# Kernel tuning notes

Measured on AMD Instinct MI355X. Metric: run time of the kernel, lower is better.

Reference implementation:

```python
import jax, jax.numpy as jnp
import numpy as np
import math

D_MODEL = 768
H = 12
D_K = D_MODEL // H


def setup_inputs() -> dict:
    key = jax.random.key(0)
    ks = jax.random.split(key, 12)
    B, S = 2, 2048
    q = jax.random.normal(ks[0], (B, S, D_MODEL), dtype=jnp.float32)
    k = jax.random.normal(ks[1], (B, S, D_MODEL), dtype=jnp.float32)
    v = jax.random.normal(ks[2], (B, S, D_MODEL), dtype=jnp.float32)
    mask = jax.random.randint(ks[3], (1, 1, S, S), 0, 2, dtype=jnp.int32)
    scale = 1.0 / math.sqrt(D_MODEL)
    w_q = jax.random.normal(ks[4], (D_MODEL, D_MODEL), dtype=jnp.float32) * scale
    b_q = jnp.zeros((D_MODEL,), dtype=jnp.float32)
    w_k = jax.random.normal(ks[5], (D_MODEL, D_MODEL), dtype=jnp.float32) * scale
    b_k = jnp.zeros((D_MODEL,), dtype=jnp.float32)
    w_v = jax.random.normal(ks[6], (D_MODEL, D_MODEL), dtype=jnp.float32) * scale
    b_v = jnp.zeros((D_MODEL,), dtype=jnp.float32)
    w_o = jax.random.normal(ks[7], (D_MODEL, D_MODEL), dtype=jnp.float32) * scale
    b_o = jnp.zeros((D_MODEL,), dtype=jnp.float32)
    return {"q": q, "k": k, "v": v, "mask": mask,
            "w_q": w_q, "b_q": b_q, "w_k": w_k, "b_k": b_k,
            "w_v": w_v, "b_v": b_v, "w_o": w_o, "b_o": b_o}


def reference(q, k, v, mask, w_q, b_q, w_k, b_k, w_v, b_v, w_o, b_o):
    B, S, _ = q.shape
    # torch nn.Linear: y = x @ W^T + b
    qp = (q @ w_q.T + b_q).reshape(B, S, H, D_K).transpose(0, 2, 1, 3)  # [B,H,S,Dk]
    kp = (k @ w_k.T + b_k).reshape(B, S, H, D_K).transpose(0, 2, 1, 3)
    vp = (v @ w_v.T + b_v).reshape(B, S, H, D_K).transpose(0, 2, 1, 3)
    # full [B,H,S,S] score matrix (the memory-bound round-trip)
    scores = jnp.einsum('bhqd,bhkd->bhqk', qp, kp) / math.sqrt(D_K)
    scores = jnp.where(mask == 0, jnp.float32(-1e9), scores)
    attn = jax.nn.softmax(scores, axis=-1)
    x = jnp.einsum('bhqk,bhkd->bhqd', attn, vp)  # [B,H,S,Dk]
    x = x.transpose(0, 2, 1, 3).reshape(B, S, H * D_K)
    return x @ w_o.T + b_o
```

## Files before the change

### kernel.cpp

```cpp
#include <hip/hip_runtime.h>
#include <hip/hip_bf16.h>

typedef __attribute__((ext_vector_type(8))) __bf16 bf16x8;
typedef __attribute__((ext_vector_type(8))) short short8;
typedef __attribute__((ext_vector_type(4))) float f32x4;
typedef __attribute__((ext_vector_type(4))) ushort us4;

#define LOG2E 1.44269504088896f

static __device__ __forceinline__ ushort f2bf(float f) {
  union { float f; unsigned u; } x; x.f = f;
  unsigned r = x.u + 0x7fffu + ((x.u >> 16) & 1u);
  return (ushort)(r >> 16);
}

static __device__ __forceinline__ void gll16(const ushort* g, ushort* l) {
  __builtin_amdgcn_global_load_lds(
      (const __attribute__((address_space(1))) unsigned*)g,
      (__attribute__((address_space(3))) unsigned*)l, 16, 0, 0);
}

#define NQ 3145728u
#define NW 589824u
__global__ __launch_bounds__(256)
void cvt_all(const float* __restrict__ q, const float* __restrict__ k,
             const float* __restrict__ v,
             const float* __restrict__ wq, const float* __restrict__ wk,
             const float* __restrict__ wv, const float* __restrict__ wo,
             ushort* __restrict__ dst)
{
  size_t i = ((size_t)blockIdx.x * 256 + threadIdx.x) * 4;
  const float* src; size_t off;
  if (i < NQ)            { src = q; off = i; }
  else if (i < 2u * NQ)  { src = k; off = i - NQ; }
  else if (i < 3u * NQ)  { src = v; off = i - 2u * NQ; }
  else {
    size_t j = i - 3u * NQ;
    unsigned wsel = (unsigned)(j / NW);
    off = j % NW;
    src = (wsel == 0) ? wq : (wsel == 1) ? wk : (wsel == 2) ? wv : wo;
  }
  f32x4 x = *(const f32x4*)(src + off);
  us4 o;
#pragma unroll
  for (int t = 0; t < 4; t++) o[t] = f2bf(x[t]);
  *(us4*)(dst + i) = o;
}

template<int MODE>
static __device__ __forceinline__ void gemm_core(const ushort* __restrict__ A,
                                                 const ushort* __restrict__ Wrow0,
                                                 const float* __restrict__ bias0,
                                                 void* __restrict__ outv,
                                                 int m0, int c0)
{
  constexpr int K = 768;
  __shared__ ushort As[128 * 32];
  __shared__ ushort Bs[128 * 32];
  const int tid  = threadIdx.x;
  const int lane = tid & 63;
  const int wid  = tid >> 6;
  const int wr = (wid >> 1) * 64;
  const int wc = (wid & 1) * 64;

  f32x4 acc[4][4];
#pragma unroll
  for (int i = 0; i < 4; i++)
#pragma unroll
    for (int j = 0; j < 4; j++) acc[i][j] = f32x4{0.f, 0.f, 0.f, 0.f};

  const int srow = wid * 16 + (lane >> 2);
  const int scol = (lane & 3) * 8;
  const ushort* gA0 = A     + (size_t)(m0 + srow) * K + scol;
  const ushort* gA1 = gA0 + (size_t)64 * K;
  const ushort* gB0 = Wrow0 + (size_t)srow * K + scol;
  const ushort* gB1 = gB0 + (size_t)64 * K;
  ushort* lA0 = &As[srow * 32 + scol];
  ushort* lA1 = &As[(srow + 64) * 32 + scol];
  ushort* lB0 = &Bs[srow * 32 + scol];
  ushort* lB1 = &Bs[(srow + 64) * 32 + scol];

  const int fr  = lane & 15;
  const int kg8 = (lane >> 4) * 8;

  for (int kt = 0; kt < K; kt += 32) {
    __syncthreads();
    gll16(gA0 + kt, lA0);
    gll16(gA1 + kt, lA1);
    gll16(gB0 + kt, lB0);
    gll16(gB1 + kt, lB1);
    __syncthreads();

    bf16x8 af[4], wf[4];
#pragma unroll
    for (int i = 0; i < 4; i++) af[i] = *(const bf16x8*)&As[(wr + i * 16 + fr) * 32 + kg8];
#pragma unroll
    for (int j = 0; j < 4; j++) wf[j] = *(const bf16x8*)&Bs[(wc + j * 16 + fr) * 32 + kg8];
#pragma unroll
    for (int i = 0; i < 4; i++)
#pragma unroll
      for (int j = 0; j < 4; j++)
        acc[i][j] = __builtin_amdgcn_mfma_f32_16x16x32_bf16(af[i], wf[j], acc[i][j], 0, 0, 0);
  }

#pragma unroll
  for (int i = 0; i < 4; i++) {
#pragma unroll
    for (int j = 0; j < 4; j++) {
#pragma unroll
      for (int r = 0; r < 4; r++) {
        int m  = m0 + wr + i * 16 + (lane >> 4) * 4 + r;
        int lc = wc + j * 16 + fr;
        float val = acc[i][j][r] + bias0[lc];
        if (MODE == 0) {
          int nn = c0 + lc;
          int hh = nn >> 6, dk = nn & 63;
          ((ushort*)outv)[(((size_t)(m >> 11) * 12 + hh) * 2048 + (m & 2047)) * 64 + dk] = f2bf(val);
        } else {
          ((float*)outv)[(size_t)m * 768 + c0 + lc] = val;
        }
      }
    }
  }
}

__global__ __launch_bounds__(256)
void qkv_gemm2(const ushort* __restrict__ CV,
               const float* __restrict__ bq, const float* __restrict__ bk,
               const float* __restrict__ bv,
               ushort* __restrict__ Qp, ushort* __restrict__ Kp, ushort* __restrict__ Vp)
{
  const int m0 = blockIdx.x * 128;
  const int n0 = blockIdx.y * 128;
  const int proj = n0 / 768;
  const int c0 = n0 - proj * 768;
  const ushort* A  = CV + (size_t)proj * NQ;
  const ushort* Wc = CV + (size_t)3 * NQ;
  const float* bias = (proj == 0) ? bq : (proj == 1) ? bk : bv;
  ushort* O = (proj == 0) ? Qp : (proj == 1) ? Kp : Vp;
  gemm_core<0>(A, Wc + (size_t)n0 * 768, bias + c0, O, m0, c0);
}

__global__ __launch_bounds__(256)
void o_gemm2(const ushort* __restrict__ X, const ushort* __restrict__ Wo,
             const float* __restrict__ bo, float* __restrict__ out)
{
  const int m0 = blockIdx.x * 128;
  const int n0 = blockIdx.y * 128;
  gemm_core<1>(X, Wo + (size_t)n0 * 768, bo + n0, out, m0, n0);
}

__global__ __launch_bounds__(256)
void attn_kernel(const ushort* __restrict__ Qp, const ushort* __restrict__ Kp,
                 const ushort* __restrict__ Vp, const int* __restrict__ mask,
                 ushort* __restrict__ X)
{
  constexpr int S = 2048;
  __shared__ ushort Ks[64][72];
  __shared__ ushort Vt[64][72];
  __shared__ ushort Ps[4][16][72];

  const int tid  = threadIdx.x;
  const int lane = tid & 63;
  const int w    = tid >> 6;
  const int qb   = blockIdx.x;
  const int bh   = blockIdx.y;
  const int b    = bh / 12, h = bh % 12;

  const ushort* Qb = Qp + (size_t)bh * S * 64;
  const ushort* Kb = Kp + (size_t)bh * S * 64;
  const ushort* Vb = Vp + (size_t)bh * S * 64;

  const int q0  = qb * 64;
  const int fr  = lane & 15;
  const int kg8 = (lane >> 4) * 8;

  const int qrow = q0 + w * 16 + fr;
  bf16x8 qf[2];
  qf[0] = *(const bf16x8*)&Qb[(size_t)qrow * 64 + kg8];
  qf[1] = *(const bf16x8*)&Qb[(size_t)qrow * 64 + 32 + kg8];

  float m_r[4] = {-1e9f, -1e9f, -1e9f, -1e9f};
  float l_r[4] = {0.f, 0.f, 0.f, 0.f};
  f32x4 accO[4];
#pragma unroll
  for (int ni = 0; ni < 4; ni++) accO[ni] = f32x4{0.f, 0.f, 0.f, 0.f};

  const int skey = tid >> 2;
  const int sc0  = (tid & 3) * 16;
  const size_t mrow_base = (size_t)(q0 + w * 16 + (lane >> 4) * 4) * S;

  for (int k0 = 0; k0 < S; k0 += 64) {
    short8 kv0 = *(const short8*)&Kb[(size_t)(k0 + skey) * 64 + sc0];
    short8 kv1 = *(const short8*)&Kb[(size_t)(k0 + skey) * 64 + sc0 + 8];
    short8 vv0 = *(const short8*)&Vb[(size_t)(k0 + skey) * 64 + sc0];
    short8 vv1 = *(const short8*)&Vb[(size_t)(k0 + skey) * 64 + sc0 + 8];
    __syncthreads();
    *(short8*)&Ks[skey][sc0]     = kv0;
    *(short8*)&Ks[skey][sc0 + 8] = kv1;
#pragma unroll
    for (int i = 0; i < 8; i++) {
      Vt[sc0 + i][skey]     = (ushort)vv0[i];
      Vt[sc0 + 8 + i][skey] = (ushort)vv1[i];
    }
    __syncthreads();

    f32x4 sc4[4];
#pragma unroll
    for (int ni = 0; ni < 4; ni++) {
      bf16x8 kf0 = *(const bf16x8*)&Ks[ni * 16 + fr][kg8];
      bf16x8 kf1 = *(const bf16x8*)&Ks[ni * 16 + fr][32 + kg8];
      f32x4 c = {0.f, 0.f, 0.f, 0.f};
      c = __builtin_amdgcn_mfma_f32_16x16x32_bf16(qf[0], kf0, c, 0, 0, 0);
      c = __builtin_amdgcn_mfma_f32_16x16x32_bf16(qf[1], kf1, c, 0, 0, 0);
      sc4[ni] = c;
    }

    float p[4][4];
#pragma unroll
    for (int r = 0; r < 4; r++) {
#pragma unroll
      for (int ni = 0; ni < 4; ni++) {
        int mk = mask[mrow_base + (size_t)r * S + k0 + ni * 16 + fr];
        float s = sc4[ni][r] * 0.125f;
        p[ni][r] = mk ? s : -1e9f;
      }
    }

#pragma unroll
    for (int r = 0; r < 4; r++) {
      float mx = fmaxf(fmaxf(p[0][r], p[1][r]), fmaxf(p[2][r], p[3][r]));
      mx = fmaxf(mx, __shfl_xor(mx, 1));
      mx = fmaxf(mx, __shfl_xor(mx, 2));
      mx = fmaxf(mx, __shfl_xor(mx, 4));
      mx = fmaxf(mx, __shfl_xor(mx, 8));
      float mn = fmaxf(m_r[r], mx);
      float al = exp2f((m_r[r] - mn) * LOG2E);
      m_r[r] = mn;
      float ls = 0.f;
#pragma unroll
      for (int ni = 0; ni < 4; ni++) {
        float e = exp2f((p[ni][r] - mn) * LOG2E);
        p[ni][r] = e;
        ls += e;
      }
      ls += __shfl_xor(ls, 1);
      ls += __shfl_xor(ls, 2);
      ls += __shfl_xor(ls, 4);
      ls += __shfl_xor(ls, 8);
      l_r[r] = l_r[r] * al + ls;
#pragma unroll
      for (int ni = 0; ni < 4; ni++) accO[ni][r] *= al;
    }

#pragma unroll
    for (int r = 0; r < 4; r++)
#pragma unroll
      for (int ni = 0; ni < 4; ni++)
        Ps[w][(lane >> 4) * 4 + r][ni * 16 + fr] = f2bf(p[ni][r]);

#pragma unroll
    for (int ks = 0; ks < 2; ks++) {
      bf16x8 pf = *(const bf16x8*)&Ps[w][fr][ks * 32 + kg8];
#pragma unroll
      for (int ni = 0; ni < 4; ni++) {
        bf16x8 vf = *(const bf16x8*)&Vt[ni * 16 + fr][ks * 32 + kg8];
        accO[ni] = __builtin_amdgcn_mfma_f32_16x16x32_bf16(pf, vf, accO[ni], 0, 0, 0);
      }
    }
  }

#pragma unroll
  for (int ni = 0; ni < 4; ni++) {
#pragma unroll
    for (int r = 0; r < 4; r++) {
      int qq = q0 + w * 16 + (lane >> 4) * 4 + r;
      float o = accO[ni][r] / l_r[r];
      X[((size_t)b * S + qq) * 768 + h * 64 + ni * 16 + fr] = f2bf(o);
    }
  }
}

extern "C" void kernel_launch(void* const* d_in, const int* in_sizes, int n_in,
                              void* d_out, int out_size, void* d_ws, size_t ws_size,
                              hipStream_t stream) {
  const float* q  = (const float*)d_in[0];
  const float* k  = (const float*)d_in[1];
  const float* v  = (const float*)d_in[2];
  const int* mask = (const int*)d_in[3];
  const float* wq = (const float*)d_in[4];
  const float* bq = (const float*)d_in[5];
  const float* wk = (const float*)d_in[6];
  const float* bk = (const float*)d_in[7];
  const float* wv = (const float*)d_in[8];
  const float* bv = (const float*)d_in[9];
  const float* wo = (const float*)d_in[10];
  const float* bo = (const float*)d_in[11];
  float* out = (float*)d_out;

  ushort* CV = (ushort*)d_ws;
  ushort* Qp = CV + (size_t)3 * NQ + (size_t)4 * NW;
  ushort* Kp = Qp + NQ;
  ushort* Vp = Kp + NQ;
  ushort* Xb = Vp + NQ;

  cvt_all<<<11520, 256, 0, stream>>>(q, k, v, wq, wk, wv, wo, CV);
  qkv_gemm2<<<dim3(32, 18), dim3(256), 0, stream>>>(CV, bq, bk, bv, Qp, Kp, Vp);
  attn_kernel<<<dim3(32, 24), dim3(256), 0, stream>>>(Qp, Kp, Vp, mask, Xb);
  o_gemm2<<<dim3(32, 6), dim3(256), 0, stream>>>(Xb, CV + (size_t)3 * NQ + (size_t)3 * NW, bo, out);
}
```

Measured before the change: 278.1 us.

## Bit-pack mask, widen attention KV tile to 128 with register prefetch

Adds a mask_pack kernel that ballots the int32 mask into 64-bit words. The attention kernel then reads bits instead of int32 values, which cuts mask traffic by a large factor. The attention loop now handles 128 keys per iteration and prefetches the next K/V tile into registers while computing the current one. It also applies a lazy softmax max-rescale with an 11.5 threshold and a pre-multiplied log2 scale, uses a packed bf16 convert, and swizzles block indices so heads in the same wave of blocks share the mask. The cost is an extra kernel launch and reuse of the CV workspace for the mask buffer; this reuse is safe only because qkv_gemm2 runs before mask_pack overwrites it. The lazy rescale also changes numerics slightly.

After: 264.1 us. -5.0%, faster.

```diff
diff --git a/kernel.cpp b/kernel.cpp
--- a/kernel.cpp
+++ b/kernel.cpp
@@ -4,14 +4,20 @@
 typedef __attribute__((ext_vector_type(8))) __bf16 bf16x8;
 typedef __attribute__((ext_vector_type(8))) short short8;
 typedef __attribute__((ext_vector_type(4))) float f32x4;
-typedef __attribute__((ext_vector_type(4))) ushort us4;
 
 #define LOG2E 1.44269504088896f
+#define SCL (0.125f * 1.44269504088896f)
 
 static __device__ __forceinline__ ushort f2bf(float f) {
   union { float f; unsigned u; } x; x.f = f;
   unsigned r = x.u + 0x7fffu + ((x.u >> 16) & 1u);
   return (ushort)(r >> 16);
+}
+
+static __device__ __forceinline__ unsigned cvt_pk_bf16(float a, float b) {
+  unsigned r;
+  asm("v_cvt_pk_bf16_f32 %0, %1, %2" : "=v"(r) : "v"(a), "v"(b));
+  return r;
 }
 
 static __device__ __forceinline__ void gll16(const ushort* g, ushort* l) {
@@ -41,10 +47,20 @@
     src = (wsel == 0) ? wq : (wsel == 1) ? wk : (wsel == 2) ? wv : wo;
   }
   f32x4 x = *(const f32x4*)(src + off);
-  us4 o;
-#pragma unroll
-  for (int t = 0; t < 4; t++) o[t] = f2bf(x[t]);
-  *(us4*)(dst + i) = o;
+  uint2 o;
+  o.x = cvt_pk_bf16(x[0], x[1]);
+  o.y = cvt_pk_bf16(x[2], x[3]);
+  *(uint2*)(dst + i) = o;
+}
+
+__global__ __launch_bounds__(256)
+void mask_pack(const int* __restrict__ mask, unsigned long long* __restrict__ mb)
+{
+  size_t gw = (size_t)blockIdx.x * 4 + (threadIdx.x >> 6);
+  int lane = threadIdx.x & 63;
+  int mk = mask[gw * 64 + lane];
+  unsigned long long bits = __ballot(mk != 0);
+  if (lane == 0) mb[gw] = bits;
 }
 
 template<int MODE>
@@ -150,22 +166,24 @@
   gemm_core<1>(X, Wo + (size_t)n0 * 768, bo + n0, out, m0, n0);
 }
 
-__global__ __launch_bounds__(256)
+__global__ __launch_bounds__(256, 3)
 void attn_kernel(const ushort* __restrict__ Qp, const ushort* __restrict__ Kp,
-                 const ushort* __restrict__ Vp, const int* __restrict__ mask,
+                 const ushort* __restrict__ Vp,
+                 const unsigned long long* __restrict__ mb,
                  ushort* __restrict__ X)
 {
   constexpr int S = 2048;
-  __shared__ ushort Ks[64][72];
-  __shared__ ushort Vt[64][72];
-  __shared__ ushort Ps[4][16][72];
+  __shared__ ushort Ks[128][72];
+  __shared__ ushort Vt[64][136];
+  __shared__ ushort Ps[4][16][136];
 
   const int tid  = threadIdx.x;
   const int lane = tid & 63;
   const int w    = tid >> 6;
-  const int qb   = blockIdx.x;
-  const int bh   = blockIdx.y;
-  const int b    = bh / 12, h = bh % 12;
+  const int bid  = blockIdx.x;
+  const int bh = (bid & 7) + 8 * (bid >> 8);
+  const int qb = (bid >> 3) & 31;
+  const int b = bh / 12, h = bh % 12;
 
   const ushort* Qb = Qp + (size_t)bh * S * 64;
   const ushort* Kb = Kp + (size_t)bh * S * 64;
@@ -173,12 +191,13 @@
 
   const int q0  = qb * 64;
   const int fr  = lane & 15;
-  const int kg8 = (lane >> 4) * 8;
+  const int g   = lane >> 4;
+  const int kg8 = g * 8;
+  const int qrow4 = q0 + w * 16 + g * 4;
 
   const int qrow = q0 + w * 16 + fr;
-  bf16x8 qf[2];
-  qf[0] = *(const bf16x8*)&Qb[(size_t)qrow * 64 + kg8];
-  qf[1] = *(const bf16x8*)&Qb[(size_t)qrow * 64 + 32 + kg8];
+  bf16x8 qf0 = *(const bf16x8*)&Qb[(size_t)qrow * 64 + kg8];
+  bf16x8 qf1 = *(const bf16x8*)&Qb[(size_t)qrow * 64 + 32 + kg8];
 
   float m_r[4] = {-1e9f, -1e9f, -1e9f, -1e9f};
   float l_r[4] = {0.f, 0.f, 0.f, 0.f};
@@ -188,79 +207,104 @@
 
   const int skey = tid >> 2;
   const int sc0  = (tid & 3) * 16;
-  const size_t mrow_base = (size_t)(q0 + w * 16 + (lane >> 4) * 4) * S;
-
-  for (int k0 = 0; k0 < S; k0 += 64) {
-    short8 kv0 = *(const short8*)&Kb[(size_t)(k0 + skey) * 64 + sc0];
-    short8 kv1 = *(const short8*)&Kb[(size_t)(k0 + skey) * 64 + sc0 + 8];
-    short8 vv0 = *(const short8*)&Vb[(size_t)(k0 + skey) * 64 + sc0];
-    short8 vv1 = *(const short8*)&Vb[(size_t)(k0 + skey) * 64 + sc0 + 8];
+  const uint4* mb4 = (const uint4*)mb;
+
+  short8 kr0, kr1, kr2, kr3, vr0, vr1, vr2, vr3;
+  {
+    const ushort* kb = Kb + (size_t)skey * 64 + sc0;
+    const ushort* vb = Vb + (size_t)skey * 64 + sc0;
+    kr0 = *(const short8*)kb;          kr1 = *(const short8*)(kb + 8);
+    kr2 = *(const short8*)(kb + 4096); kr3 = *(const short8*)(kb + 4104);
+    vr0 = *(const short8*)vb;          vr1 = *(const short8*)(vb + 8);
+    vr2 = *(const short8*)(vb + 4096); vr3 = *(const short8*)(vb + 4104);
+  }
+
+  for (int tt = 0; tt < 16; tt++) {
     __syncthreads();
-    *(short8*)&Ks[skey][sc0]     = kv0;
-    *(short8*)&Ks[skey][sc0 + 8] = kv1;
+    *(short8*)&Ks[skey][sc0]          = kr0;
+    *(short8*)&Ks[skey][sc0 + 8]      = kr1;
+    *(short8*)&Ks[64 + skey][sc0]     = kr2;
+    *(short8*)&Ks[64 + skey][sc0 + 8] = kr3;
 #pragma unroll
     for (int i = 0; i < 8; i++) {
-      Vt[sc0 + i][skey]     = (ushort)vv0[i];
-      Vt[sc0 + 8 + i][skey] = (ushort)vv1[i];
+      Vt[sc0 + i][skey]          = (ushort)vr0[i];
+      Vt[sc0 + 8 + i][skey]      = (ushort)vr1[i];
+      Vt[sc0 + i][64 + skey]     = (ushort)vr2[i];
+      Vt[sc0 + 8 + i][64 + skey] = (ushort)vr3[i];
     }
     __syncthreads();
 
-    f32x4 sc4[4];
-#pragma unroll
-    for (int ni = 0; ni < 4; ni++) {
+    uint4 mB[4];
+#pragma unroll
+    for (int r = 0; r < 4; r++)
+      mB[r] = mb4[(size_t)(qrow4 + r) * 16 + tt];
+
+    if (tt < 15) {
+      const ushort* kb = Kb + (size_t)((tt + 1) * 128 + skey) * 64 + sc0;
+      const ushort* vb = Vb + (size_t)((tt + 1) * 128 + skey) * 64 + sc0;
+      kr0 = *(const short8*)kb;          kr1 = *(const short8*)(kb + 8);
+      kr2 = *(const short8*)(kb + 4096); kr3 = *(const short8*)(kb + 4104);
+      vr0 = *(const short8*)vb;          vr1 = *(const short8*)(vb + 8);
+      vr2 = *(const short8*)(vb + 4096); vr3 = *(const short8*)(vb + 4104);
+    }
+
+    f32x4 sc8[8];
+#pragma unroll
+    for (int ni = 0; ni < 8; ni++) {
       bf16x8 kf0 = *(const bf16x8*)&Ks[ni * 16 + fr][kg8];
       bf16x8 kf1 = *(const bf16x8*)&Ks[ni * 16 + fr][32 + kg8];
       f32x4 c = {0.f, 0.f, 0.f, 0.f};
-      c = __builtin_amdgcn_mfma_f32_16x16x32_bf16(qf[0], kf0, c, 0, 0, 0);
-      c = __builtin_amdgcn_mfma_f32_16x16x32_bf16(qf[1], kf1, c, 0, 0, 0);
-      sc4[ni] = c;
-    }
-
-    float p[4][4];
+      c = __builtin_amdgcn_mfma_f32_16x16x32_bf16(qf0, kf0, c, 0, 0, 0);
+      c = __builtin_amdgcn_mfma_f32_16x16x32_bf16(qf1, kf1, c, 0, 0, 0);
+      sc8[ni] = c;
+    }
+
 #pragma unroll
     for (int r = 0; r < 4; r++) {
-#pragma unroll
-      for (int ni = 0; ni < 4; ni++) {
-        int mk = mask[mrow_base + (size_t)r * S + k0 + ni * 16 + fr];
-        float s = sc4[ni][r] * 0.125f;
-        p[ni][r] = mk ? s : -1e9f;
-      }
-    }
-
-#pragma unroll
-    for (int r = 0; r < 4; r++) {
-      float mx = fmaxf(fmaxf(p[0][r], p[1][r]), fmaxf(p[2][r], p[3][r]));
+      float praw[8];
+#pragma unroll
+      for (int ni = 0; ni < 8; ni++) praw[ni] = sc8[ni][r] * SCL;
+      float mx = fmaxf(fmaxf(fmaxf(praw[0], praw[1]), fmaxf(praw[2], praw[3])),
+                       fmaxf(fmaxf(praw[4], praw[5]), fmaxf(praw[6], praw[7])));
       mx = fmaxf(mx, __shfl_xor(mx, 1));
       mx = fmaxf(mx, __shfl_xor(mx, 2));
       mx = fmaxf(mx, __shfl_xor(mx, 4));
       mx = fmaxf(mx, __shfl_xor(mx, 8));
-      float mn = fmaxf(m_r[r], mx);
-      float al = exp2f((m_r[r] - mn) * LOG2E);
-      m_r[r] = mn;
+      if (mx > m_r[r] + 11.5f) {
+        float al = exp2f(m_r[r] - mx);
+        m_r[r] = mx;
+        l_r[r] *= al;
+#pragma unroll
+        for (int ni = 0; ni < 4; ni++) accO[ni][r] *= al;
+      }
+      const float mr = m_r[r];
+      unsigned sx = mB[r].x >> fr, sy = mB[r].y >> fr,
+               sz = mB[r].z >> fr, sw = mB[r].w >> fr;
+      unsigned bits[8] = { sx & 1u, (sx >> 16) & 1u, sy & 1u, (sy >> 16) & 1u,
+                           sz & 1u, (sz >> 16) & 1u, sw & 1u, (sw >> 16) & 1u };
+      float e[8];
       float ls = 0.f;
 #pragma unroll
-      for (int ni = 0; ni < 4; ni++) {
-        float e = exp2f((p[ni][r] - mn) * LOG2E);
-        p[ni][r] = e;
-        ls += e;
+      for (int ni = 0; ni < 8; ni++) {
+        float t = exp2f(praw[ni] - mr);
+        t = bits[ni] ? t : 0.f;
+        e[ni] = t; ls += t;
       }
       ls += __shfl_xor(ls, 1);
       ls += __shfl_xor(ls, 2);
       ls += __shfl_xor(ls, 4);
       ls += __shfl_xor(ls, 8);
-      l_r[r] = l_r[r] * al + ls;
-#pragma unroll
-      for (int ni = 0; ni < 4; ni++) accO[ni][r] *= al;
-    }
-
-#pragma unroll
-    for (int r = 0; r < 4; r++)
-#pragma unroll
-      for (int ni = 0; ni < 4; ni++)
-        Ps[w][(lane >> 4) * 4 + r][ni * 16 + fr] = f2bf(p[ni][r]);
-
-#pragma unroll
-    for (int ks = 0; ks < 2; ks++) {
+      l_r[r] += ls;
+#pragma unroll
+      for (int a = 0; a < 4; a++) {
+        unsigned pk = cvt_pk_bf16(e[2 * a], e[2 * a + 1]);
+        Ps[w][g * 4 + r][a * 32 + fr]      = (ushort)pk;
+        Ps[w][g * 4 + r][a * 32 + 16 + fr] = (ushort)(pk >> 16);
+      }
+    }
+
+#pragma unroll
+    for (int ks = 0; ks < 4; ks++) {
       bf16x8 pf = *(const bf16x8*)&Ps[w][fr][ks * 32 + kg8];
 #pragma unroll
       for (int ni = 0; ni < 4; ni++) {
@@ -270,12 +314,15 @@
     }
   }
 
+  float inv[4];
+#pragma unroll
+  for (int r = 0; r < 4; r++) inv[r] = 1.f / l_r[r];
 #pragma unroll
   for (int ni = 0; ni < 4; ni++) {
 #pragma unroll
     for (int r = 0; r < 4; r++) {
-      int qq = q0 + w * 16 + (lane >> 4) * 4 + r;
-      float o = accO[ni][r] / l_r[r];
+      int qq = qrow4 + r;
+      float o = accO[ni][r] * inv[r];
       X[((size_t)b * S + qq) * 768 + h * 64 + ni * 16 + fr] = f2bf(o);
     }
   }
@@ -303,9 +350,11 @@
   ushort* Kp = Qp + NQ;
   ushort* Vp = Kp + NQ;
   ushort* Xb = Vp + NQ;
+  unsigned long long* mbuf = (unsigned long long*)CV;
 
   cvt_all<<<11520, 256, 0, stream>>>(q, k, v, wq, wk, wv, wo, CV);
   qkv_gemm2<<<dim3(32, 18), dim3(256), 0, stream>>>(CV, bq, bk, bv, Qp, Kp, Vp);
-  attn_kernel<<<dim3(32, 24), dim3(256), 0, stream>>>(Qp, Kp, Vp, mask, Xb);
+  mask_pack<<<16384, 256, 0, stream>>>(mask, mbuf);
+  attn_kernel<<<768, 256, 0, stream>>>(Qp, Kp, Vp, mbuf, Xb);
   o_gemm2<<<dim3(32, 6), dim3(256), 0, stream>>>(Xb, CV + (size_t)3 * NQ + (size_t)3 * NW, bo, out);
 }
```
